# Optimization experiments

Hardware: AMD Instinct MI355X
Metric: run time of the kernel (lower is better)

Reference implementation:

```python
import jax, jax.numpy as jnp
import numpy as np

B, L, CIN, COUT, HEADS = 8, 2048, 256, 256, 4
HD = COUT // HEADS
NEG_SLOPE = 0.2


def setup_inputs() -> dict:
    key = jax.random.key(0)
    k1, k2, k3, k4, k5 = jax.random.split(key, 5)
    x = jax.random.normal(k1, (B, L, CIN), dtype=jnp.float32)
    adj_mask = jax.random.randint(k2, (B, L, L), 0, 2) > 0  # bool [B,L,L]
    W = jax.random.normal(k3, (COUT, CIN), dtype=jnp.float32) * (1.0 / np.sqrt(CIN))
    att_src = jax.random.normal(k4, (1, HEADS, 1, HD), dtype=jnp.float32) * 0.1
    att_dst = jax.random.normal(k5, (1, HEADS, 1, HD), dtype=jnp.float32) * 0.1
    return {"x": x, "adj_mask": adj_mask, "W": W, "att_src": att_src, "att_dst": att_dst}


def reference(x, adj_mask, W, att_src, att_dst):
    Bb, Ll, _ = x.shape
    # linear projection (no bias), split heads: [B, H, L, D]
    h = jnp.einsum('blc,oc->blo', x, W).reshape(Bb, Ll, HEADS, HD).transpose(0, 2, 1, 3)
    # additive GAT scores
    a_src = jnp.sum(h * att_src, axis=-1, keepdims=True)          # [B,H,L,1]
    a_dst = jnp.sum(h * att_dst, axis=-1, keepdims=True)          # [B,H,L,1]
    e = a_src + jnp.swapaxes(a_dst, 2, 3)                          # [B,H,L,L]
    e = jnp.where(e >= 0, e, NEG_SLOPE * e)                        # leaky relu
    fill = jnp.finfo(e.dtype).min
    e = jnp.where(adj_mask[:, None, :, :], e, fill)                # mask non-edges
    alpha = jax.nn.softmax(e, axis=-1)                             # [B,H,L,L]
    # dropout is identity in eval/reference mode
    out = jnp.einsum('bhij,bhjd->bhid', alpha, h)                  # [B,H,L,D]
    return out.transpose(0, 2, 1, 3).reshape(Bb, Ll, COUT)
```

## Files before the change

### kernel.cpp

```cpp
#include <hip/hip_runtime.h>

#define B_ 8
#define L_ 2048
#define CIN_ 256
#define COUT_ 256
#define HEADS_ 4
#define HD_ 64
#define NEG_SLOPE_ 0.2f
#define LOG2E_ 1.4426950408889634f

#define TI 32
#define TJ 64
#define NJT (L_ / TJ)

typedef __attribute__((ext_vector_type(4))) float f32x4;
typedef __attribute__((ext_vector_type(8))) __bf16 bf16x8;
typedef __attribute__((ext_vector_type(4))) __bf16 bf16x4;


__global__ __launch_bounds__(256, 4)
void pack_kernel(const int* __restrict__ adj, unsigned long long* __restrict__ abitsT) {
  const size_t wid = ((size_t)blockIdx.x * 256 + threadIdx.x) >> 6;
  const int lane = threadIdx.x & 63;
  const int* p = adj + wid * 256 + lane;
  unsigned long long b0 = __ballot(p[0]   != 0);
  unsigned long long b1 = __ballot(p[64]  != 0);
  unsigned long long b2 = __ballot(p[128] != 0);
  unsigned long long b3 = __ballot(p[192] != 0);
  if (lane == 0) {
    const size_t row = wid >> 3;
    const int jw0 = (int)(wid & 7) * 4;
    const size_t bb = row >> 11, l = row & 2047;
    unsigned long long* dst = abitsT + (bb << 16) + l;
    dst[(size_t)(jw0 + 0) << 11] = b0;
    dst[(size_t)(jw0 + 1) << 11] = b1;
    dst[(size_t)(jw0 + 2) << 11] = b2;
    dst[(size_t)(jw0 + 3) << 11] = b3;
  }
}

__global__ __launch_bounds__(256, 2)
void proj_kernel(const float* __restrict__ x, const float* __restrict__ W,
                 const float* __restrict__ att_src, const float* __restrict__ att_dst,
                 __bf16* __restrict__ hF, float2* __restrict__ aE,
                 float2* __restrict__ aF) {
  __shared__ __align__(16) __bf16 Wl[COUT_][80];
  __shared__ __align__(16) __bf16 Al[2][2][512];

  const int tid = threadIdx.x;
  const int r0 = blockIdx.x * TI;
  const int b  = r0 >> 11;
  const int l0 = r0 & (L_ - 1);

  const int w = tid >> 6, lane = tid & 63, col = lane & 15, q = lane >> 4;
  const int si = tid >> 3, soct = tid & 7;
  const int wn = tid >> 2, wkq = tid & 3;

  f32x4 acc[2][4];
#pragma unroll
  for (int mt = 0; mt < 2; ++mt)
#pragma unroll
    for (int nt = 0; nt < 4; ++nt) acc[mt][nt] = (f32x4)0.f;

  for (int kc = 0; kc < CIN_ / 64; ++kc) {
    __syncthreads();
#pragma unroll
    for (int rg = 0; rg < 4; ++rg) {
      const int row = rg * 64 + wn;
      const float4* ws = (const float4*)(W + (size_t)row * CIN_ + kc * 64 + wkq * 16);
#pragma unroll
      for (int u = 0; u < 4; ++u) {
        float4 f = ws[u];
        bf16x4 v;
        v[0] = (__bf16)f.x; v[1] = (__bf16)f.y; v[2] = (__bf16)f.z; v[3] = (__bf16)f.w;
        *(bf16x4*)&Wl[row][wkq * 16 + u * 4] = v;
      }
    }
    {
      const float4* xs = (const float4*)(x + (size_t)(r0 + si) * CIN_ + kc * 64 + soct * 8);
      float4 f0 = xs[0], f1 = xs[1];
      bf16x8 v;
      v[0] = (__bf16)f0.x; v[1] = (__bf16)f0.y; v[2] = (__bf16)f0.z; v[3] = (__bf16)f0.w;
      v[4] = (__bf16)f1.x; v[5] = (__bf16)f1.y; v[6] = (__bf16)f1.z; v[7] = (__bf16)f1.w;
      *(bf16x8*)&Al[si >> 4][soct >> 2][(((soct & 3) << 4) + (si & 15)) << 3] = v;
    }
    __syncthreads();

    bf16x8 af[2][2], bfr[2][4];
#pragma unroll
    for (int mt = 0; mt < 2; ++mt)
#pragma unroll
      for (int kt = 0; kt < 2; ++kt)
        af[mt][kt] = *(const bf16x8*)&Al[mt][kt][lane << 3];
#pragma unroll
    for (int kt = 0; kt < 2; ++kt)
#pragma unroll
      for (int nt = 0; nt < 4; ++nt)
        bfr[kt][nt] = *(const bf16x8*)&Wl[w * 64 + nt * 16 + col][kt * 32 + q * 8];
#pragma unroll
    for (int kt = 0; kt < 2; ++kt)
#pragma unroll
      for (int mt = 0; mt < 2; ++mt)
#pragma unroll
        for (int nt = 0; nt < 4; ++nt)
          acc[mt][nt] = __builtin_amdgcn_mfma_f32_16x16x32_bf16(
              af[mt][kt], bfr[kt][nt], acc[mt][nt], 0, 0, 0);
  }

  float asv[4], adv[4];
#pragma unroll
  for (int nt = 0; nt < 4; ++nt) {
    asv[nt] = att_src[w * 64 + nt * 16 + col];
    adv[nt] = att_dst[w * 64 + nt * 16 + col];
  }
#pragma unroll
  for (int mt = 0; mt < 2; ++mt)
#pragma unroll
    for (int reg = 0; reg < 4; ++reg) {
      float s = 0.f, d = 0.f;
#pragma unroll
      for (int nt = 0; nt < 4; ++nt) {
        s = fmaf(acc[mt][nt][reg], asv[nt], s);
        d = fmaf(acc[mt][nt][reg], adv[nt], d);
      }
      s += __shfl_xor(s, 1, 64); d += __shfl_xor(d, 1, 64);
      s += __shfl_xor(s, 2, 64); d += __shfl_xor(d, 2, 64);
      s += __shfl_xor(s, 4, 64); d += __shfl_xor(d, 4, 64);
      s += __shfl_xor(s, 8, 64); d += __shfl_xor(d, 8, 64);
      if (col == 0) {
        int il = mt * 16 + q * 4 + reg;
        const size_t idx = ((size_t)(b * HEADS_ + w) << 11) + l0 + il;
        float2 ev, fv;
        ev.x = __builtin_exp2f(s * LOG2E_);
        ev.y = __builtin_exp2f(s * (LOG2E_ * NEG_SLOPE_));
        fv.x = __builtin_exp2f(d * LOG2E_);
        fv.y = __builtin_exp2f(d * (LOG2E_ * NEG_SLOPE_));
        aE[idx] = ev;
        aF[idx] = fv;
      }
    }

  {
    const int jt_p = l0 >> 6;
    const int kt_p = (l0 >> 5) & 1;
    const int qhi = q >> 1, qlo = q & 1;
#pragma unroll
    for (int mt = 0; mt < 2; ++mt) {
      const int qp = mt * 2 + qhi;
#pragma unroll
      for (int nt = 0; nt < 4; ++nt) {
        bf16x4 v;
        v[0] = (__bf16)acc[mt][nt][0];
        v[1] = (__bf16)acc[mt][nt][1];
        v[2] = (__bf16)acc[mt][nt][2];
        v[3] = (__bf16)acc[mt][nt][3];
        const size_t off =
            ((((size_t)(b * HEADS_ + w) * 32 + jt_p) * 2 + kt_p) * 4 + nt) * 512 +
            (qp * 16 + col) * 8 + qlo * 4;
        *(bf16x4*)(hF + off) = v;
      }
    }
  }
}

__global__ __launch_bounds__(256, 2)
void attn_kernel(const __bf16* __restrict__ hF, const float2* __restrict__ aE,
                 const float2* __restrict__ aF,
                 const unsigned long long* __restrict__ abitsT,
                 float* __restrict__ out) {
  const int tid = threadIdx.x;
  const int b  = blockIdx.x & 7;
  const int i0 = (blockIdx.x >> 3) * 32;

  const int w = tid >> 6, lane = tid & 63, col = lane & 15, q = lane >> 4;

  const size_t hl = (size_t)(b * HEADS_ + w);
  const float2 EE[2] = {aE[(hl << 11) + i0 + col],
                        aE[(hl << 11) + i0 + 16 + col]};
  const float* afb = (const float*)(aF + (hl << 11)) + q * 16;
  const __bf16* hb = hF + hl * 131072 + lane * 8;
  const unsigned long long* mb = abitsT + ((size_t)b << 16) + i0 + col;

  bf16x8 bones;
#pragma unroll
  for (int e = 0; e < 8; ++e) bones[e] = (__bf16)1.0f;

  f32x4 acc[2][4], accl[2];
#pragma unroll
  for (int mt = 0; mt < 2; ++mt) {
    accl[mt] = (f32x4)0.f;
#pragma unroll
    for (int nt = 0; nt < 4; ++nt) acc[mt][nt] = (f32x4)0.f;
  }

  unsigned long long cm0 = mb[0], cm1 = mb[16];

  for (int jt = 0; jt < NJT; ++jt) {
    bf16x8 cb[2][4];
#pragma unroll
    for (int kt = 0; kt < 2; ++kt)
#pragma unroll
      for (int nt = 0; nt < 4; ++nt)
        cb[kt][nt] = *(const bf16x8*)(hb + jt * 4096 + (kt * 4 + nt) * 512);
    float cf[2][16];
#pragma unroll
    for (int kt = 0; kt < 2; ++kt)
#pragma unroll
      for (int u = 0; u < 4; ++u)
        *(float4*)&cf[kt][u * 4] =
            *(const float4*)(afb + jt * 128 + kt * 64 + u * 4);

    const int jn = (jt < NJT - 1) ? jt + 1 : jt;
    const unsigned long long nm0 = mb[(size_t)jn << 11];
    const unsigned long long nm1 = mb[((size_t)jn << 11) + 16];

    bf16x8 av[2][2];
#pragma unroll
    for (int mt = 0; mt < 2; ++mt) {
      const unsigned long long bw = mt ? cm1 : cm0;
      const float Ex = EE[mt].x, Ey = EE[mt].y;
#pragma unroll
      for (int kt = 0; kt < 2; ++kt) {
        const unsigned int tsh = ((unsigned int)(bw >> (kt * 32))) >> (q * 8);
#pragma unroll
        for (int e = 0; e < 8; ++e) {
          const float m1 = Ex * cf[kt][2 * e];
          const float m2 = Ey * cf[kt][2 * e + 1];
          const float pm = fmaxf(m1, m2);
          const float p = (tsh & (1u << e)) ? pm : 0.f;
          av[mt][kt][e] = (__bf16)p;
        }
      }
    }

#pragma unroll
    for (int kt = 0; kt < 2; ++kt)
#pragma unroll
      for (int mt = 0; mt < 2; ++mt) {
#pragma unroll
        for (int nt = 0; nt < 4; ++nt)
          acc[mt][nt] = __builtin_amdgcn_mfma_f32_16x16x32_bf16(
              av[mt][kt], cb[kt][nt], acc[mt][nt], 0, 0, 0);
        accl[mt] = __builtin_amdgcn_mfma_f32_16x16x32_bf16(
            av[mt][kt], bones, accl[mt], 0, 0, 0);
      }

    cm0 = nm0; cm1 = nm1;
  }

#pragma unroll
  for (int mt = 0; mt < 2; ++mt)
#pragma unroll
    for (int reg = 0; reg < 4; ++reg) {
      const int m = q * 4 + reg;
      const float linv = 1.0f / accl[mt][reg];
      const size_t orow =
          ((size_t)(b * L_ + i0 + mt * 16 + m)) * COUT_ + w * 64;
#pragma unroll
      for (int nt = 0; nt < 4; ++nt)
        out[orow + nt * 16 + col] = acc[mt][nt][reg] * linv;
    }
}

extern "C" void kernel_launch(void* const* d_in, const int* in_sizes, int n_in,
                              void* d_out, int out_size, void* d_ws, size_t ws_size,
                              hipStream_t stream) {
  const float* x       = (const float*)d_in[0];
  const int*   adj     = (const int*)d_in[1];
  const float* W       = (const float*)d_in[2];
  const float* att_src = (const float*)d_in[3];
  const float* att_dst = (const float*)d_in[4];
  float* out = (float*)d_out;

  char* ws = (char*)d_ws;
  __bf16* hF = (__bf16*)ws;
  float2* aE = (float2*)(ws + (8u << 20));
  float2* aF = (float2*)(ws + (9u << 20));
  unsigned long long* abitsT =
      (unsigned long long*)(ws + (10u << 20));

  pack_kernel<<<(B_ * L_ * (L_ / 256)) / 4, 256, 0, stream>>>(adj, abitsT);
  proj_kernel<<<(B_ * L_) / TI, 256, 0, stream>>>(x, W, att_src, att_dst, hF, aE, aF);
  attn_kernel<<<B_ * (L_ / 32), 256, 0, stream>>>(hF, aE, aF, abitsT, out);
}
```

Before: 265.3 us.

## Fuse mask packing into projection and split attention key range across wave halves

The adjacency bit-packing kernel is folded into the projection kernel, with each wave looping over 64 packing work-items before the GEMM. This removes one launch and lets the memory-bound packing share a grid with the projection. The attention kernel now uses 512-thread blocks in which two wave groups each process half of the key tiles per head. Their partial numerators and row sums are combined through shared memory before normalisation, which doubles parallelism per output tile at the cost of extra LDS traffic and a block-wide barrier.

```diff
diff --git a/kernel.cpp b/kernel.cpp
--- a/kernel.cpp
+++ b/kernel.cpp
@@ -18,30 +18,10 @@
 typedef __attribute__((ext_vector_type(4))) __bf16 bf16x4;
 
 
-__global__ __launch_bounds__(256, 4)
-void pack_kernel(const int* __restrict__ adj, unsigned long long* __restrict__ abitsT) {
-  const size_t wid = ((size_t)blockIdx.x * 256 + threadIdx.x) >> 6;
-  const int lane = threadIdx.x & 63;
-  const int* p = adj + wid * 256 + lane;
-  unsigned long long b0 = __ballot(p[0]   != 0);
-  unsigned long long b1 = __ballot(p[64]  != 0);
-  unsigned long long b2 = __ballot(p[128] != 0);
-  unsigned long long b3 = __ballot(p[192] != 0);
-  if (lane == 0) {
-    const size_t row = wid >> 3;
-    const int jw0 = (int)(wid & 7) * 4;
-    const size_t bb = row >> 11, l = row & 2047;
-    unsigned long long* dst = abitsT + (bb << 16) + l;
-    dst[(size_t)(jw0 + 0) << 11] = b0;
-    dst[(size_t)(jw0 + 1) << 11] = b1;
-    dst[(size_t)(jw0 + 2) << 11] = b2;
-    dst[(size_t)(jw0 + 3) << 11] = b3;
-  }
-}
-
 __global__ __launch_bounds__(256, 2)
 void proj_kernel(const float* __restrict__ x, const float* __restrict__ W,
                  const float* __restrict__ att_src, const float* __restrict__ att_dst,
+                 const int* __restrict__ adj, unsigned long long* __restrict__ abitsT,
                  __bf16* __restrict__ hF, float2* __restrict__ aE,
                  float2* __restrict__ aF) {
   __shared__ __align__(16) __bf16 Wl[COUT_][80];
@@ -55,6 +35,28 @@
   const int w = tid >> 6, lane = tid & 63, col = lane & 15, q = lane >> 4;
   const int si = tid >> 3, soct = tid & 7;
   const int wn = tid >> 2, wkq = tid & 3;
+
+  {
+    const size_t wid0 = (size_t)blockIdx.x * 256 + (size_t)w * 64;
+    for (int c = 0; c < 64; ++c) {
+      const size_t wid = wid0 + c;
+      const int* p = adj + wid * 256 + lane;
+      unsigned long long b0 = __ballot(p[0]   != 0);
+      unsigned long long b1 = __ballot(p[64]  != 0);
+      unsigned long long b2 = __ballot(p[128] != 0);
+      unsigned long long b3 = __ballot(p[192] != 0);
+      if (lane == 0) {
+        const size_t row = wid >> 3;
+        const int jw0 = (int)(wid & 7) * 4;
+        const size_t bb = row >> 11, l = row & 2047;
+        unsigned long long* dst = abitsT + (bb << 16) + l;
+        dst[(size_t)(jw0 + 0) << 11] = b0;
+        dst[(size_t)(jw0 + 1) << 11] = b1;
+        dst[(size_t)(jw0 + 2) << 11] = b2;
+        dst[(size_t)(jw0 + 3) << 11] = b3;
+      }
+    }
+  }
 
   f32x4 acc[2][4];
 #pragma unroll
@@ -163,18 +165,23 @@
   }
 }
 
-__global__ __launch_bounds__(256, 2)
+__global__ __launch_bounds__(512, 4)
 void attn_kernel(const __bf16* __restrict__ hF, const float2* __restrict__ aE,
                  const float2* __restrict__ aF,
                  const unsigned long long* __restrict__ abitsT,
                  float* __restrict__ out) {
+  __shared__ __align__(16) float comb[HEADS_][64][40];
+
   const int tid = threadIdx.x;
   const int b  = blockIdx.x & 7;
   const int i0 = (blockIdx.x >> 3) * 32;
 
   const int w = tid >> 6, lane = tid & 63, col = lane & 15, q = lane >> 4;
-
-  const size_t hl = (size_t)(b * HEADS_ + w);
+  const int hh = w & 3;
+  const int jh = w >> 2;
+  const int jt0 = jh * (NJT / 2), jt1 = jt0 + NJT / 2;
+
+  const size_t hl = (size_t)(b * HEADS_ + hh);
   const float2 EE[2] = {aE[(hl << 11) + i0 + col],
                         aE[(hl << 11) + i0 + 16 + col]};
   const float* afb = (const float*)(aF + (hl << 11)) + q * 16;
@@ -193,9 +200,10 @@
     for (int nt = 0; nt < 4; ++nt) acc[mt][nt] = (f32x4)0.f;
   }
 
-  unsigned long long cm0 = mb[0], cm1 = mb[16];
-
-  for (int jt = 0; jt < NJT; ++jt) {
+  unsigned long long cm0 = mb[(size_t)jt0 << 11];
+  unsigned long long cm1 = mb[((size_t)jt0 << 11) + 16];
+
+  for (int jt = jt0; jt < jt1; ++jt) {
     bf16x8 cb[2][4];
 #pragma unroll
     for (int kt = 0; kt < 2; ++kt)
@@ -210,7 +218,7 @@
         *(float4*)&cf[kt][u * 4] =
             *(const float4*)(afb + jt * 128 + kt * 64 + u * 4);
 
-    const int jn = (jt < NJT - 1) ? jt + 1 : jt;
+    const int jn = (jt < jt1 - 1) ? jt + 1 : jt;
     const unsigned long long nm0 = mb[(size_t)jn << 11];
     const unsigned long long nm1 = mb[((size_t)jn << 11) + 16];
 
@@ -248,18 +256,35 @@
     cm0 = nm0; cm1 = nm1;
   }
 
-#pragma unroll
-  for (int mt = 0; mt < 2; ++mt)
-#pragma unroll
-    for (int reg = 0; reg < 4; ++reg) {
-      const int m = q * 4 + reg;
-      const float linv = 1.0f / accl[mt][reg];
-      const size_t orow =
-          ((size_t)(b * L_ + i0 + mt * 16 + m)) * COUT_ + w * 64;
+  if (jh == 1) {
+#pragma unroll
+    for (int mt = 0; mt < 2; ++mt)
 #pragma unroll
       for (int nt = 0; nt < 4; ++nt)
-        out[orow + nt * 16 + col] = acc[mt][nt][reg] * linv;
-    }
+        *(f32x4*)&comb[hh][lane][mt * 16 + nt * 4] = acc[mt][nt];
+    *(f32x4*)&comb[hh][lane][32] = accl[0];
+    *(f32x4*)&comb[hh][lane][36] = accl[1];
+  }
+  __syncthreads();
+  if (jh == 0) {
+#pragma unroll
+    for (int mt = 0; mt < 2; ++mt) {
+      const f32x4 lo = accl[mt] + *(const f32x4*)&comb[hh][lane][32 + mt * 4];
+#pragma unroll
+      for (int reg = 0; reg < 4; ++reg) {
+        const int m = q * 4 + reg;
+        const float linv = 1.0f / lo[reg];
+        const size_t orow =
+            ((size_t)(b * L_ + i0 + mt * 16 + m)) * COUT_ + hh * 64;
+#pragma unroll
+        for (int nt = 0; nt < 4; ++nt) {
+          const float v =
+              acc[mt][nt][reg] + comb[hh][lane][mt * 16 + nt * 4 + reg];
+          out[orow + nt * 16 + col] = v * linv;
+        }
+      }
+    }
+  }
 }
 
 extern "C" void kernel_launch(void* const* d_in, const int* in_sizes, int n_in,
@@ -279,7 +304,7 @@
   unsigned long long* abitsT =
       (unsigned long long*)(ws + (10u << 20));
 
-  pack_kernel<<<(B_ * L_ * (L_ / 256)) / 4, 256, 0, stream>>>(adj, abitsT);
-  proj_kernel<<<(B_ * L_) / TI, 256, 0, stream>>>(x, W, att_src, att_dst, hF, aE, aF);
-  attn_kernel<<<B_ * (L_ / 32), 256, 0, stream>>>(hF, aE, aF, abitsT, out);
+  proj_kernel<<<(B_ * L_) / TI, 256, 0, stream>>>(x, W, att_src, att_dst,
+                                                  adj, abitsT, hF, aE, aF);
+  attn_kernel<<<B_ * (L_ / 32), 512, 0, stream>>>(hF, aE, aF, abitsT, out);
 }
```

Result: slower. 324.9 us (+22.5%).

## Halve attention row tile to 16 rows and double occupancy

Applied to the files above, without the earlier changes.

The attention kernel now handles 16 query rows per block instead of 32. The grid doubles and launch bounds rise from 2 to 4 blocks per CU. The mask prefetch across iterations is dropped, and the B-operand loads move inside the kt loop to cut register pressure. The cost is that each block reuses the loaded h/aF tiles across half as many rows, which doubles global/L2 traffic for those operands, and there is no longer mask prefetching.

```diff
diff --git a/kernel.cpp b/kernel.cpp
--- a/kernel.cpp
+++ b/kernel.cpp
@@ -163,20 +163,19 @@
   }
 }
 
-__global__ __launch_bounds__(256, 2)
+__global__ __launch_bounds__(256, 4)
 void attn_kernel(const __bf16* __restrict__ hF, const float2* __restrict__ aE,
                  const float2* __restrict__ aF,
                  const unsigned long long* __restrict__ abitsT,
                  float* __restrict__ out) {
   const int tid = threadIdx.x;
   const int b  = blockIdx.x & 7;
-  const int i0 = (blockIdx.x >> 3) * 32;
+  const int i0 = (blockIdx.x >> 3) * 16;
 
   const int w = tid >> 6, lane = tid & 63, col = lane & 15, q = lane >> 4;
 
   const size_t hl = (size_t)(b * HEADS_ + w);
-  const float2 EE[2] = {aE[(hl << 11) + i0 + col],
-                        aE[(hl << 11) + i0 + 16 + col]};
+  const float2 EE = aE[(hl << 11) + i0 + col];
   const float* afb = (const float*)(aF + (hl << 11)) + q * 16;
   const __bf16* hb = hF + hl * 131072 + lane * 8;
   const unsigned long long* mb = abitsT + ((size_t)b << 16) + i0 + col;
@@ -185,81 +184,55 @@
 #pragma unroll
   for (int e = 0; e < 8; ++e) bones[e] = (__bf16)1.0f;
 
-  f32x4 acc[2][4], accl[2];
-#pragma unroll
-  for (int mt = 0; mt < 2; ++mt) {
-    accl[mt] = (f32x4)0.f;
-#pragma unroll
-    for (int nt = 0; nt < 4; ++nt) acc[mt][nt] = (f32x4)0.f;
-  }
-
-  unsigned long long cm0 = mb[0], cm1 = mb[16];
+  f32x4 acc[4], accl;
+  accl = (f32x4)0.f;
+#pragma unroll
+  for (int nt = 0; nt < 4; ++nt) acc[nt] = (f32x4)0.f;
+
+  const float Ex = EE.x, Ey = EE.y;
 
   for (int jt = 0; jt < NJT; ++jt) {
-    bf16x8 cb[2][4];
-#pragma unroll
-    for (int kt = 0; kt < 2; ++kt)
-#pragma unroll
-      for (int nt = 0; nt < 4; ++nt)
-        cb[kt][nt] = *(const bf16x8*)(hb + jt * 4096 + (kt * 4 + nt) * 512);
-    float cf[2][16];
-#pragma unroll
-    for (int kt = 0; kt < 2; ++kt)
+    const unsigned long long cm = mb[(size_t)jt << 11];
+#pragma unroll
+    for (int kt = 0; kt < 2; ++kt) {
+      bf16x8 cb0 = *(const bf16x8*)(hb + jt * 4096 + (kt * 4 + 0) * 512);
+      bf16x8 cb1 = *(const bf16x8*)(hb + jt * 4096 + (kt * 4 + 1) * 512);
+      bf16x8 cb2 = *(const bf16x8*)(hb + jt * 4096 + (kt * 4 + 2) * 512);
+      bf16x8 cb3 = *(const bf16x8*)(hb + jt * 4096 + (kt * 4 + 3) * 512);
+      float cf[16];
 #pragma unroll
       for (int u = 0; u < 4; ++u)
-        *(float4*)&cf[kt][u * 4] =
+        *(float4*)&cf[u * 4] =
             *(const float4*)(afb + jt * 128 + kt * 64 + u * 4);
 
-    const int jn = (jt < NJT - 1) ? jt + 1 : jt;
-    const unsigned long long nm0 = mb[(size_t)jn << 11];
-    const unsigned long long nm1 = mb[((size_t)jn << 11) + 16];
-
-    bf16x8 av[2][2];
-#pragma unroll
-    for (int mt = 0; mt < 2; ++mt) {
-      const unsigned long long bw = mt ? cm1 : cm0;
-      const float Ex = EE[mt].x, Ey = EE[mt].y;
-#pragma unroll
-      for (int kt = 0; kt < 2; ++kt) {
-        const unsigned int tsh = ((unsigned int)(bw >> (kt * 32))) >> (q * 8);
-#pragma unroll
-        for (int e = 0; e < 8; ++e) {
-          const float m1 = Ex * cf[kt][2 * e];
-          const float m2 = Ey * cf[kt][2 * e + 1];
-          const float pm = fmaxf(m1, m2);
-          const float p = (tsh & (1u << e)) ? pm : 0.f;
-          av[mt][kt][e] = (__bf16)p;
-        }
-      }
-    }
-
-#pragma unroll
-    for (int kt = 0; kt < 2; ++kt)
-#pragma unroll
-      for (int mt = 0; mt < 2; ++mt) {
-#pragma unroll
-        for (int nt = 0; nt < 4; ++nt)
-          acc[mt][nt] = __builtin_amdgcn_mfma_f32_16x16x32_bf16(
-              av[mt][kt], cb[kt][nt], acc[mt][nt], 0, 0, 0);
-        accl[mt] = __builtin_amdgcn_mfma_f32_16x16x32_bf16(
-            av[mt][kt], bones, accl[mt], 0, 0, 0);
-      }
-
-    cm0 = nm0; cm1 = nm1;
-  }
-
-#pragma unroll
-  for (int mt = 0; mt < 2; ++mt)
-#pragma unroll
-    for (int reg = 0; reg < 4; ++reg) {
-      const int m = q * 4 + reg;
-      const float linv = 1.0f / accl[mt][reg];
-      const size_t orow =
-          ((size_t)(b * L_ + i0 + mt * 16 + m)) * COUT_ + w * 64;
-#pragma unroll
-      for (int nt = 0; nt < 4; ++nt)
-        out[orow + nt * 16 + col] = acc[mt][nt][reg] * linv;
-    }
+      const unsigned int tsh = ((unsigned int)(cm >> (kt * 32))) >> (q * 8);
+      bf16x8 av;
+#pragma unroll
+      for (int e = 0; e < 8; ++e) {
+        const float m1 = Ex * cf[2 * e];
+        const float m2 = Ey * cf[2 * e + 1];
+        const float pm = fmaxf(m1, m2);
+        const float p = (tsh & (1u << e)) ? pm : 0.f;
+        av[e] = (__bf16)p;
+      }
+
+      acc[0] = __builtin_amdgcn_mfma_f32_16x16x32_bf16(av, cb0, acc[0], 0, 0, 0);
+      acc[1] = __builtin_amdgcn_mfma_f32_16x16x32_bf16(av, cb1, acc[1], 0, 0, 0);
+      acc[2] = __builtin_amdgcn_mfma_f32_16x16x32_bf16(av, cb2, acc[2], 0, 0, 0);
+      acc[3] = __builtin_amdgcn_mfma_f32_16x16x32_bf16(av, cb3, acc[3], 0, 0, 0);
+      accl   = __builtin_amdgcn_mfma_f32_16x16x32_bf16(av, bones, accl, 0, 0, 0);
+    }
+  }
+
+#pragma unroll
+  for (int reg = 0; reg < 4; ++reg) {
+    const int m = q * 4 + reg;
+    const float linv = 1.0f / accl[reg];
+    const size_t orow = ((size_t)(b * L_ + i0 + m)) * COUT_ + w * 64;
+#pragma unroll
+    for (int nt = 0; nt < 4; ++nt)
+      out[orow + nt * 16 + col] = acc[nt][reg] * linv;
+  }
 }
 
 extern "C" void kernel_launch(void* const* d_in, const int* in_sizes, int n_in,
@@ -281,5 +254,5 @@
 
   pack_kernel<<<(B_ * L_ * (L_ / 256)) / 4, 256, 0, stream>>>(adj, abitsT);
   proj_kernel<<<(B_ * L_) / TI, 256, 0, stream>>>(x, W, att_src, att_dst, hF, aE, aF);
-  attn_kernel<<<B_ * (L_ / 32), 256, 0, stream>>>(hF, aE, aF, abitsT, out);
-}
+  attn_kernel<<<B_ * (L_ / 16), 256, 0, stream>>>(hF, aE, aF, abitsT, out);
+}
```

Measured after the change: 287.1 us. 1.08x slower.
